# Kernel optimization log

Measured on AMD Instinct MI355X. Metric: run time of the kernel, lower is better.

Reference implementation:

```python
import jax, jax.numpy as jnp
import numpy as np
import math

N = 100000      # num vertices
M = 50000       # num hyperedges
NNZ = 800000    # incidence entries
F_IN = 128
NHID = 128
NCLS = 40
DEPTH = 4
ALPHA = 0.1     # restart_alpha
LAMDA = 0.5


def setup_inputs() -> dict:
    key = jax.random.key(0)
    ks = jax.random.split(key, 8)
    x = jax.random.normal(ks[0], (N, F_IN), jnp.float32)
    vertex = jax.random.randint(ks[1], (NNZ,), 0, N)
    edges = jax.random.randint(ks[2], (NNZ,), 0, M)
    s0 = 1.0 / np.sqrt(F_IN)
    sh = 1.0 / np.sqrt(NHID)
    W0 = jax.random.uniform(ks[3], (F_IN, NHID), jnp.float32, -s0, s0)
    b0 = jax.random.uniform(ks[4], (NHID,), jnp.float32, -s0, s0)
    Ws = jax.random.uniform(ks[5], (DEPTH, NHID, NHID), jnp.float32, -sh, sh)
    Wout = jax.random.uniform(ks[6], (NHID, NCLS), jnp.float32, -sh, sh)
    bout = jax.random.uniform(ks[7], (NCLS,), jnp.float32, -sh, sh)
    return {"x": x, "W0": W0, "b0": b0, "Ws": Ws, "Wout": Wout,
            "bout": bout, "vertex": vertex, "edges": edges}


def reference(x, W0, b0, Ws, Wout, bout, vertex, edges):
    ones = jnp.ones((NNZ, 1), x.dtype)
    cnt_e = jnp.maximum(jax.ops.segment_sum(ones, edges, num_segments=M), 1.0)
    cnt_v = jnp.maximum(jax.ops.segment_sum(ones, vertex, num_segments=N), 1.0)

    x = jax.nn.relu(x @ W0 + b0)
    x0 = x
    for i in range(DEPTH):
        beta = math.log(LAMDA / (i + 1) + 1.0)
        # vertex -> edge mean aggregation
        Xve = x[vertex]                                          # [NNZ, NHID]
        Xe = jax.ops.segment_sum(Xve, edges, num_segments=M) / cnt_e
        # edge -> vertex mean aggregation
        Xev = Xe[edges]                                          # [NNZ, NHID]
        Xv = jax.ops.segment_sum(Xev, vertex, num_segments=N) / cnt_v
        # L2 row-normalize with detached scale (use_norm=True)
        norm = jnp.linalg.norm(Xv, axis=1, keepdims=True)
        scale = jax.lax.stop_gradient(jnp.where(norm > 0, 1.0 / norm, 0.0))
        Xv = Xv * scale
        # alpha/beta residual blend (UniGCNII)
        Xi = (1.0 - ALPHA) * Xv + ALPHA * x0
        x = jax.nn.relu((1.0 - beta) * Xi + beta * (Xi @ Ws[i]))
    return x @ Wout + bout
```

## Files before the change

### kernel.cpp

```cpp
#include <hip/hip_runtime.h>

#define NV 100000
#define NE 50000
#define NNZ_C 800000
#define CAP_E 64
#define CAP_V 48
#define NB_E 391
#define NB_V 782
#define CAPB_E 2560
#define CAPB_V 1408
#define OVF_CAP 810000
#define T_ITEMS 4096
#define N_TILES ((NNZ_C + T_ITEMS - 1) / T_ITEMS)

typedef unsigned int uint32;
typedef unsigned short u16;
typedef u16 u16x8 __attribute__((ext_vector_type(8)));
typedef short short8 __attribute__((ext_vector_type(8)));
typedef float floatx16 __attribute__((ext_vector_type(16)));

__device__ __forceinline__ float bf2f(u16 h) {
  return __uint_as_float(((uint32)h) << 16);
}
__device__ __forceinline__ u16 f2bf(float f) {
  uint32 u = __float_as_uint(f);
  u += 0x7FFF + ((u >> 16) & 1);
  return (u16)(u >> 16);
}


__global__ void zero_misc(int* __restrict__ cur, int n,
                          u16* __restrict__ dummyX, u16* __restrict__ dummyXe) {
  int i = blockIdx.x * blockDim.x + threadIdx.x;
  if (i < n) cur[i] = 0;
  if (i < 128) { dummyX[i] = 0; dummyXe[i] = 0; }
}


__global__ __launch_bounds__(256) void scatter_binned(const int* __restrict__ vertex,
                                                      const int* __restrict__ edges,
                                                      int* __restrict__ curE,
                                                      int* __restrict__ curV,
                                                      int* __restrict__ ovfCnt,
                                                      uint32* __restrict__ pairE,
                                                      uint32* __restrict__ pairV,
                                                      uint2* __restrict__ ovfE,
                                                      uint2* __restrict__ ovfV) {
  __shared__ int histE[NB_E], baseE[NB_E];
  __shared__ int histV[NB_V], baseV[NB_V];
  int t = threadIdx.x;
  for (int tile = blockIdx.x; tile < N_TILES; tile += gridDim.x) {
    for (int b = t; b < NB_E; b += 256) histE[b] = 0;
    for (int b = t; b < NB_V; b += 256) histV[b] = 0;
    __syncthreads();
    int base = tile * T_ITEMS;
    int ev[16], vv[16], rE[16], rV[16];
    #pragma unroll
    for (int i = 0; i < 16; i++) {
      int k = base + t + i * 256;
      if (k < NNZ_C) {
        ev[i] = edges[k];
        vv[i] = vertex[k];
        rE[i] = atomicAdd(&histE[ev[i] >> 7], 1);
        rV[i] = atomicAdd(&histV[vv[i] >> 7], 1);
      }
    }
    __syncthreads();
    for (int b = t; b < NB_E; b += 256) {
      int h = histE[b];
      baseE[b] = h ? atomicAdd(&curE[b], h) : 0;
    }
    for (int b = t; b < NB_V; b += 256) {
      int h = histV[b];
      baseV[b] = h ? atomicAdd(&curV[b], h) : 0;
    }
    __syncthreads();
    #pragma unroll
    for (int i = 0; i < 16; i++) {
      int k = base + t + i * 256;
      if (k < NNZ_C) {
        uint32 e = (uint32)ev[i], v = (uint32)vv[i];
        uint32 pkE = ((e & 127u) << 25) | v;
        uint32 pkV = ((v & 127u) << 25) | e;
        int pE = baseE[e >> 7] + rE[i];
        if (pE < CAPB_E) pairE[(size_t)(e >> 7) * CAPB_E + pE] = pkE;
        else { int op = atomicAdd(&ovfCnt[0], 1); if (op < OVF_CAP) ovfE[op] = make_uint2(e >> 7, pkE); }
        int pV = baseV[v >> 7] + rV[i];
        if (pV < CAPB_V) pairV[(size_t)(v >> 7) * CAPB_V + pV] = pkV;
        else { int op = atomicAdd(&ovfCnt[1], 1); if (op < OVF_CAP) ovfV[op] = make_uint2(v >> 7, pkV); }
      }
    }
    __syncthreads();
  }
}

__global__ __launch_bounds__(256) void expand(const uint32* __restrict__ pairs,
                                              const int* __restrict__ cur, int capb,
                                              const uint2* __restrict__ ovf,
                                              const int* __restrict__ ovfCnt,
                                              int* __restrict__ items, int cap,
                                              int* __restrict__ cnt, int nKeys,
                                              int P, int dummy) {
  __shared__ int lcnt[128];
  int b = blockIdx.x, t = threadIdx.x;
  if (t < 128) lcnt[t] = 0;
  __syncthreads();
  int n = min(cur[b], capb);
  const uint32* p = pairs + (size_t)b * capb;
  for (int i = t; i < n; i += 256) {
    uint32 w = p[i];
    int loc = w >> 25;
    int val = (int)(w & 0x1FFFFFFu);
    int r = atomicAdd(&lcnt[loc], 1);
    if (r < cap) items[(size_t)((b << 7) + loc) * cap + r] = val;
  }
  int novf = min(*ovfCnt, OVF_CAP);
  for (int i = t; i < novf; i += 256) {
    uint2 w = ovf[i];
    if ((int)w.x == b) {
      int loc = w.y >> 25;
      int val = (int)(w.y & 0x1FFFFFFu);
      int r = atomicAdd(&lcnt[loc], 1);
      if (r < cap) items[(size_t)((b << 7) + loc) * cap + r] = val;
    }
  }
  __syncthreads();
  if (t < 128) {
    int key = (b << 7) + t;
    if (key < nKeys) {
      int c = lcnt[t];
      cnt[key] = c;
      int cc = min(c, cap);
      int padded = min((cc + P - 1) & ~(P - 1), cap);
      for (int r = cc; r < padded; r++)
        items[(size_t)key * cap + r] = dummy;
    }
  }
}


__global__ void prep_weights(const float* __restrict__ W0, const float* __restrict__ Ws,
                             u16* __restrict__ WT) {
  int idx = blockIdx.x * blockDim.x + threadIdx.x;
  if (idx >= 5 * 16384) return;
  const float betas[4] = {0.4054651081f, 0.2231435513f, 0.1541506798f, 0.1177830357f};
  int sec = idx >> 14;
  int rc = idx & 16383;
  int n = rc >> 7, k = rc & 127;
  float v;
  if (sec == 0) {
    v = W0[k * 128 + n];
  } else {
    int i = sec - 1;
    float b = betas[i];
    v = b * Ws[i * 16384 + k * 128 + n];
    if (k == n) v += 1.0f - b;
  }
  WT[idx] = f2bf(v);
}


__global__ __launch_bounds__(256) void edge_agg(const u16* __restrict__ Xh,
                                                const int* __restrict__ cntE,
                                                const int* __restrict__ itemsE,
                                                u16* __restrict__ Xeh) {
  int g = threadIdx.x >> 4;
  int lane = threadIdx.x & 15;
  int e = blockIdx.x * 16 + g;
  int cnt = cntE[e];
  int n16 = (min(cnt, CAP_E) + 15) & ~15;
  const int* it = itemsE + (size_t)e * CAP_E;
  float acc[8] = {0.f, 0.f, 0.f, 0.f, 0.f, 0.f, 0.f, 0.f};
  for (int j = 0; j < n16; j += 16) {
    int4 i0 = *(const int4*)(it + j);
    int4 i1 = *(const int4*)(it + j + 4);
    int4 i2 = *(const int4*)(it + j + 8);
    int4 i3 = *(const int4*)(it + j + 12);
    u16x8 r0 = *(const u16x8*)(Xh + (size_t)i0.x * 128 + lane * 8);
    u16x8 r1 = *(const u16x8*)(Xh + (size_t)i0.y * 128 + lane * 8);
    u16x8 r2 = *(const u16x8*)(Xh + (size_t)i0.z * 128 + lane * 8);
    u16x8 r3 = *(const u16x8*)(Xh + (size_t)i0.w * 128 + lane * 8);
    u16x8 r4 = *(const u16x8*)(Xh + (size_t)i1.x * 128 + lane * 8);
    u16x8 r5 = *(const u16x8*)(Xh + (size_t)i1.y * 128 + lane * 8);
    u16x8 r6 = *(const u16x8*)(Xh + (size_t)i1.z * 128 + lane * 8);
    u16x8 r7 = *(const u16x8*)(Xh + (size_t)i1.w * 128 + lane * 8);
    u16x8 r8 = *(const u16x8*)(Xh + (size_t)i2.x * 128 + lane * 8);
    u16x8 r9 = *(const u16x8*)(Xh + (size_t)i2.y * 128 + lane * 8);
    u16x8 rA = *(const u16x8*)(Xh + (size_t)i2.z * 128 + lane * 8);
    u16x8 rB = *(const u16x8*)(Xh + (size_t)i2.w * 128 + lane * 8);
    u16x8 rC = *(const u16x8*)(Xh + (size_t)i3.x * 128 + lane * 8);
    u16x8 rD = *(const u16x8*)(Xh + (size_t)i3.y * 128 + lane * 8);
    u16x8 rE = *(const u16x8*)(Xh + (size_t)i3.z * 128 + lane * 8);
    u16x8 rF = *(const u16x8*)(Xh + (size_t)i3.w * 128 + lane * 8);
    #pragma unroll
    for (int q = 0; q < 8; q++) {
      float s0 = (bf2f(r0[q]) + bf2f(r1[q])) + (bf2f(r2[q]) + bf2f(r3[q]));
      float s1 = (bf2f(r4[q]) + bf2f(r5[q])) + (bf2f(r6[q]) + bf2f(r7[q]));
      float s2 = (bf2f(r8[q]) + bf2f(r9[q])) + (bf2f(rA[q]) + bf2f(rB[q]));
      float s3 = (bf2f(rC[q]) + bf2f(rD[q])) + (bf2f(rE[q]) + bf2f(rF[q]));
      acc[q] += (s0 + s1) + (s2 + s3);
    }
  }
  float inv = 1.f / fmaxf((float)cnt, 1.f);
  u16x8 o;
  #pragma unroll
  for (int q = 0; q < 8; q++) o[q] = f2bf(acc[q] * inv);
  *(u16x8*)(Xeh + (size_t)e * 128 + lane * 8) = o;
}


__global__ __launch_bounds__(256, 5) void gemm_fused(const u16* __restrict__ Xeh,
                                                     const int* __restrict__ cntV,
                                                     const int* __restrict__ itemsV,
                                                     const u16* __restrict__ x0h,
                                                     const u16* __restrict__ WT,
                                                     u16* __restrict__ Yh, int nrows) {
  __shared__ u16 As[64 * 136];
  int t = threadIdx.x;
  int row0 = blockIdx.x * 64;
  int g = t >> 4, lane = t & 15;
  #pragma unroll
  for (int pass = 0; pass < 4; pass++) {
    int r = pass * 16 + g;
    int v = row0 + r;
    float acc[8] = {0.f, 0.f, 0.f, 0.f, 0.f, 0.f, 0.f, 0.f};
    int cnt = 0;
    if (v < nrows) {
      cnt = cntV[v];
      int n8 = (min(cnt, CAP_V) + 7) & ~7;
      const int* it = itemsV + (size_t)v * CAP_V;
      for (int j = 0; j < n8; j += 8) {
        int4 e0 = *(const int4*)(it + j);
        int4 e1 = *(const int4*)(it + j + 4);
        u16x8 r0 = *(const u16x8*)(Xeh + (size_t)e0.x * 128 + lane * 8);
        u16x8 r1 = *(const u16x8*)(Xeh + (size_t)e0.y * 128 + lane * 8);
        u16x8 r2 = *(const u16x8*)(Xeh + (size_t)e0.z * 128 + lane * 8);
        u16x8 r3 = *(const u16x8*)(Xeh + (size_t)e0.w * 128 + lane * 8);
        u16x8 r4 = *(const u16x8*)(Xeh + (size_t)e1.x * 128 + lane * 8);
        u16x8 r5 = *(const u16x8*)(Xeh + (size_t)e1.y * 128 + lane * 8);
        u16x8 r6 = *(const u16x8*)(Xeh + (size_t)e1.z * 128 + lane * 8);
        u16x8 r7 = *(const u16x8*)(Xeh + (size_t)e1.w * 128 + lane * 8);
        #pragma unroll
        for (int q = 0; q < 8; q++)
          acc[q] += ((bf2f(r0[q]) + bf2f(r1[q])) + (bf2f(r2[q]) + bf2f(r3[q]))) +
                    ((bf2f(r4[q]) + bf2f(r5[q])) + (bf2f(r6[q]) + bf2f(r7[q])));
      }
    }
    float inv = 1.f / fmaxf((float)cnt, 1.f);
    float sq = 0.f;
    #pragma unroll
    for (int q = 0; q < 8; q++) { acc[q] *= inv; sq += acc[q] * acc[q]; }
    sq += __shfl_xor(sq, 1, 64);
    sq += __shfl_xor(sq, 2, 64);
    sq += __shfl_xor(sq, 4, 64);
    sq += __shfl_xor(sq, 8, 64);
    float scale = (sq > 0.f) ? rsqrtf(sq) : 0.f;
    u16x8 o = {0, 0, 0, 0, 0, 0, 0, 0};
    if (v < nrows) {
      u16x8 x0v = *(const u16x8*)(x0h + (size_t)v * 128 + lane * 8);
      #pragma unroll
      for (int q = 0; q < 8; q++)
        o[q] = f2bf(0.9f * acc[q] * scale + 0.1f * bf2f(x0v[q]));
    }
    *(u16x8*)&As[r * 136 + lane * 8] = o;
  }
  __syncthreads();

  int w = t >> 6, lane64 = t & 63;
  int l31 = lane64 & 31, kh = lane64 >> 5;
  int wr = w >> 1, wc = w & 1;
  floatx16 acc[2];
  #pragma unroll
  for (int ct = 0; ct < 2; ct++)
    #pragma unroll
    for (int q = 0; q < 16; q++) acc[ct][q] = 0.f;

  const u16* wtb0 = WT + (size_t)(wc * 64 + l31) * 128;
  const u16* wtb1 = WT + (size_t)(wc * 64 + 32 + l31) * 128;
  #pragma unroll
  for (int ks = 0; ks < 8; ks++) {
    int koff = ks * 16 + kh * 8;
    short8 b0 = *(const short8*)(wtb0 + koff);
    short8 b1 = *(const short8*)(wtb1 + koff);
    short8 a0 = *(const short8*)&As[(wr * 32 + l31) * 136 + koff];
    acc[0] = __builtin_amdgcn_mfma_f32_32x32x16_bf16(a0, b0, acc[0], 0, 0, 0);
    acc[1] = __builtin_amdgcn_mfma_f32_32x32x16_bf16(a0, b1, acc[1], 0, 0, 0);
  }
  __syncthreads();

  #pragma unroll
  for (int ct = 0; ct < 2; ct++) {
    int col = wc * 64 + ct * 32 + l31;
    #pragma unroll
    for (int reg = 0; reg < 16; reg++) {
      int row = wr * 32 + (reg & 3) + 8 * (reg >> 2) + 4 * kh;
      As[row * 136 + col] = f2bf(fmaxf(acc[ct][reg], 0.f));
    }
  }
  __syncthreads();
  #pragma unroll
  for (int i = 0; i < 4; i++) {
    int idx = t + 256 * i;
    int r = idx >> 4, c8 = idx & 15;
    if (row0 + r < nrows)
      *(u16x8*)(Yh + (size_t)(row0 + r) * 128 + c8 * 8) =
          *(const u16x8*)&As[r * 136 + c8 * 8];
  }
}

__global__ __launch_bounds__(256, 4) void gemm_first(const float* __restrict__ A,
                                                     const u16* __restrict__ WT,
                                                     const float* __restrict__ bias,
                                                     u16* __restrict__ Yh,
                                                     u16* __restrict__ Y2h, int nrows) {
  __shared__ u16 As[128 * 136];
  int t = threadIdx.x;
  int row0 = blockIdx.x * 128;
  #pragma unroll
  for (int i = 0; i < 8; i++) {
    int idx = t + 256 * i;
    int r = idx >> 4, c8 = idx & 15;
    u16x8 v = {0, 0, 0, 0, 0, 0, 0, 0};
    if (row0 + r < nrows) {
      const float* p = A + (size_t)(row0 + r) * 128 + c8 * 8;
      float4 a = *(const float4*)p;
      float4 b = *(const float4*)(p + 4);
      v[0] = f2bf(a.x); v[1] = f2bf(a.y); v[2] = f2bf(a.z); v[3] = f2bf(a.w);
      v[4] = f2bf(b.x); v[5] = f2bf(b.y); v[6] = f2bf(b.z); v[7] = f2bf(b.w);
    }
    *(u16x8*)&As[r * 136 + c8 * 8] = v;
  }
  __syncthreads();

  int w = t >> 6, lane = t & 63;
  int l31 = lane & 31, kh = lane >> 5;
  int wr = w >> 1, wc = w & 1;
  floatx16 acc[2][2];
  #pragma unroll
  for (int rt = 0; rt < 2; rt++)
    #pragma unroll
    for (int ct = 0; ct < 2; ct++)
      #pragma unroll
      for (int q = 0; q < 16; q++) acc[rt][ct][q] = 0.f;

  const u16* wtb0 = WT + (size_t)(wc * 64 + l31) * 128;
  const u16* wtb1 = WT + (size_t)(wc * 64 + 32 + l31) * 128;
  #pragma unroll
  for (int ks = 0; ks < 8; ks++) {
    int koff = ks * 16 + kh * 8;
    short8 b0 = *(const short8*)(wtb0 + koff);
    short8 b1 = *(const short8*)(wtb1 + koff);
    short8 a0 = *(const short8*)&As[(wr * 64 + l31) * 136 + koff];
    short8 a1 = *(const short8*)&As[(wr * 64 + 32 + l31) * 136 + koff];
    acc[0][0] = __builtin_amdgcn_mfma_f32_32x32x16_bf16(a0, b0, acc[0][0], 0, 0, 0);
    acc[0][1] = __builtin_amdgcn_mfma_f32_32x32x16_bf16(a0, b1, acc[0][1], 0, 0, 0);
    acc[1][0] = __builtin_amdgcn_mfma_f32_32x32x16_bf16(a1, b0, acc[1][0], 0, 0, 0);
    acc[1][1] = __builtin_amdgcn_mfma_f32_32x32x16_bf16(a1, b1, acc[1][1], 0, 0, 0);
  }
  __syncthreads();

  #pragma unroll
  for (int rt = 0; rt < 2; rt++)
    #pragma unroll
    for (int ct = 0; ct < 2; ct++) {
      int col = wc * 64 + ct * 32 + l31;
      float bv = bias[col];
      #pragma unroll
      for (int reg = 0; reg < 16; reg++) {
        int row = wr * 64 + rt * 32 + (reg & 3) + 8 * (reg >> 2) + 4 * kh;
        As[row * 136 + col] = f2bf(fmaxf(acc[rt][ct][reg] + bv, 0.f));
      }
    }
  __syncthreads();
  #pragma unroll
  for (int i = 0; i < 8; i++) {
    int idx = t + 256 * i;
    int r = idx >> 4, c8 = idx & 15;
    if (row0 + r < nrows) {
      u16x8 v = *(const u16x8*)&As[r * 136 + c8 * 8];
      *(u16x8*)(Yh + (size_t)(row0 + r) * 128 + c8 * 8) = v;
      *(u16x8*)(Y2h + (size_t)(row0 + r) * 128 + c8 * 8) = v;
    }
  }
}


__global__ __launch_bounds__(256) void gemm_out(const u16* __restrict__ Xh,
                                                const float* __restrict__ W,
                                                const float* __restrict__ bias,
                                                float* __restrict__ Y, int nrows) {
  __shared__ float xs[128][36];
  __shared__ float ws[32][44];
  int t = threadIdx.x;
  int tr = t >> 3;
  int tc = t & 7;
  int row0 = blockIdx.x * 128;
  float acc[4][5];
  #pragma unroll
  for (int i = 0; i < 4; i++)
    #pragma unroll
    for (int j = 0; j < 5; j++) acc[i][j] = 0.f;

  for (int k0 = 0; k0 < 128; k0 += 32) {
    #pragma unroll
    for (int i = 0; i < 2; i++) {
      int idx = t + 256 * i;
      int r = idx >> 2, c8 = idx & 3;
      int gr = row0 + r;
      u16x8 v = {0, 0, 0, 0, 0, 0, 0, 0};
      if (gr < nrows) v = *(const u16x8*)(Xh + (size_t)gr * 128 + k0 + c8 * 8);
      #pragma unroll
      for (int q = 0; q < 8; q++) xs[r][c8 * 8 + q] = bf2f(v[q]);
    }
    #pragma unroll
    for (int i = 0; i < 5; i++) {
      int idx = t + 256 * i;
      int r = idx / 40, c = idx % 40;
      ws[r][c] = W[(k0 + r) * 40 + c];
    }
    __syncthreads();
    #pragma unroll
    for (int kk4 = 0; kk4 < 8; kk4++) {
      float4 xv[4];
      #pragma unroll
      for (int i = 0; i < 4; i++) xv[i] = *(const float4*)&xs[tr + 32 * i][kk4 * 4];
      #pragma unroll
      for (int q = 0; q < 4; q++) {
        int kk = kk4 * 4 + q;
        float wv[5];
        #pragma unroll
        for (int j = 0; j < 5; j++) wv[j] = ws[kk][tc * 5 + j];
        #pragma unroll
        for (int i = 0; i < 4; i++) {
          float xq = ((const float*)&xv[i])[q];
          #pragma unroll
          for (int j = 0; j < 5; j++) acc[i][j] += xq * wv[j];
        }
      }
    }
    __syncthreads();
  }
  #pragma unroll
  for (int i = 0; i < 4; i++) {
    int gr = row0 + tr + 32 * i;
    if (gr >= nrows) continue;
    #pragma unroll
    for (int j = 0; j < 5; j++) {
      int c = tc * 5 + j;
      Y[(long)gr * 40 + c] = acc[i][j] + bias[c];
    }
  }
}


extern "C" void kernel_launch(void* const* d_in, const int* in_sizes, int n_in,
                              void* d_out, int out_size, void* d_ws, size_t ws_size,
                              hipStream_t stream) {
  const float* x    = (const float*)d_in[0];
  const float* W0   = (const float*)d_in[1];
  const float* b0   = (const float*)d_in[2];
  const float* Ws   = (const float*)d_in[3];
  const float* Wout = (const float*)d_in[4];
  const float* bout = (const float*)d_in[5];
  const int* vertex = (const int*)d_in[6];
  const int* edges  = (const int*)d_in[7];
  float* out = (float*)d_out;

  char* base = (char*)d_ws;
  size_t o = 0;
  auto alloc = [&](size_t bytes) -> char* {
    char* r = base + o;
    o += (bytes + 255) & ~(size_t)255;
    return r;
  };
  u16* x_curh = (u16*)alloc((size_t)(NV + 1) * 128 * 2);
  u16* x0h    = (u16*)alloc((size_t)NV * 128 * 2);
  u16* Xeh    = (u16*)alloc((size_t)(NE + 1) * 128 * 2);
  u16* WT     = (u16*)alloc((size_t)5 * 16384 * 2);
  int* cntE   = (int*)alloc((size_t)NE * 4);
  int* cntV   = (int*)alloc((size_t)NV * 4);
  int* itemsE = (int*)alloc((size_t)NE * CAP_E * 4);
  int* itemsV = (int*)alloc((size_t)NV * CAP_V * 4);
  uint32* pairE = (uint32*)alloc((size_t)NB_E * CAPB_E * 4);
  uint32* pairV = (uint32*)alloc((size_t)NB_V * CAPB_V * 4);
  uint2* ovfE  = (uint2*)alloc((size_t)OVF_CAP * 8);
  uint2* ovfV  = (uint2*)alloc((size_t)OVF_CAP * 8);
  int* curAll = (int*)alloc((size_t)(NB_E + NB_V + 2) * 4);
  int* curE = curAll;
  int* curV = curAll + NB_E;
  int* ovfCnt = curAll + NB_E + NB_V;

  int nzero = NB_E + NB_V + 2;
  zero_misc<<<(nzero + 255) / 256, 256, 0, stream>>>(curAll, nzero,
                                                     x_curh + (size_t)NV * 128,
                                                     Xeh + (size_t)NE * 128);
  scatter_binned<<<N_TILES, 256, 0, stream>>>(vertex, edges, curE, curV, ovfCnt,
                                              pairE, pairV, ovfE, ovfV);
  expand<<<NB_E, 256, 0, stream>>>(pairE, curE, CAPB_E, ovfE, ovfCnt,
                                   itemsE, CAP_E, cntE, NE, 16, NV);
  expand<<<NB_V, 256, 0, stream>>>(pairV, curV, CAPB_V, ovfV, ovfCnt + 1,
                                   itemsV, CAP_V, cntV, NV, 8, NE);
  prep_weights<<<(5 * 16384 + 255) / 256, 256, 0, stream>>>(W0, Ws, WT);

  int gblocks = (NV + 127) / 128;
  int fblocks = (NV + 63) / 64;
  gemm_first<<<gblocks, 256, 0, stream>>>(x, WT, b0, x_curh, x0h, NV);

  for (int i = 0; i < 4; i++) {
    edge_agg<<<NE / 16, 256, 0, stream>>>(x_curh, cntE, itemsE, Xeh);
    gemm_fused<<<fblocks, 256, 0, stream>>>(Xeh, cntV, itemsV, x0h,
                                            WT + (size_t)(1 + i) * 16384, x_curh, NV);
  }
  gemm_out<<<gblocks, 256, 0, stream>>>(x_curh, Wout, bout, out, NV);
}
```

Before: 481.0 us.

## Slice feature matrices into 16-column planes for cache-local gathers

Feature matrices move to a sliced layout of 8 planes, each holding 16 columns per row. Edge and vertex gathers then run per slice (blockIdx & 7), so each slice's working set (about 3.2MB for vertices) can stay in cache during the random gathers. The vertex aggregation is split out of the fused GEMM into its own kernel, which writes partial squared norms that the GEMM reduces. The cost is an extra kernel and an intermediate Xv buffer round-trip per layer. The index lists are also reread 8 times, once per slice.

```diff
diff --git a/kernel.cpp b/kernel.cpp
--- a/kernel.cpp
+++ b/kernel.cpp
@@ -12,6 +12,8 @@
 #define OVF_CAP 810000
 #define T_ITEMS 4096
 #define N_TILES ((NNZ_C + T_ITEMS - 1) / T_ITEMS)
+#define ET (NB_E)
+#define VT (NB_V)
 
 typedef unsigned int uint32;
 typedef unsigned short u16;
@@ -30,10 +32,14 @@
 
 
 __global__ void zero_misc(int* __restrict__ cur, int n,
-                          u16* __restrict__ dummyX, u16* __restrict__ dummyXe) {
+                          u16* __restrict__ Xcs, u16* __restrict__ Xes) {
   int i = blockIdx.x * blockDim.x + threadIdx.x;
   if (i < n) cur[i] = 0;
-  if (i < 128) { dummyX[i] = 0; dummyXe[i] = 0; }
+  if (i < 128) {
+    int s = i >> 4, j = i & 15;
+    Xcs[((size_t)s * (NV + 1) + NV) * 16 + j] = 0;
+    Xes[((size_t)s * (NE + 1) + NE) * 16 + j] = 0;
+  }
 }
 
 
@@ -160,38 +166,42 @@
 }
 
 
-__global__ __launch_bounds__(256) void edge_agg(const u16* __restrict__ Xh,
-                                                const int* __restrict__ cntE,
-                                                const int* __restrict__ itemsE,
-                                                u16* __restrict__ Xeh) {
-  int g = threadIdx.x >> 4;
-  int lane = threadIdx.x & 15;
-  int e = blockIdx.x * 16 + g;
+__global__ __launch_bounds__(256) void edge_agg_s(const u16* __restrict__ Xcs,
+                                                  const int* __restrict__ cntE,
+                                                  const int* __restrict__ itemsE,
+                                                  u16* __restrict__ Xes) {
+  int s = blockIdx.x & 7;
+  int tile = blockIdx.x >> 3;
+  int t = threadIdx.x;
+  int p = t >> 1, half = t & 1;
+  int e = tile * 128 + p;
+  if (e >= NE) return;
   int cnt = cntE[e];
   int n16 = (min(cnt, CAP_E) + 15) & ~15;
   const int* it = itemsE + (size_t)e * CAP_E;
+  const u16* src = Xcs + (size_t)s * (NV + 1) * 16 + half * 8;
   float acc[8] = {0.f, 0.f, 0.f, 0.f, 0.f, 0.f, 0.f, 0.f};
   for (int j = 0; j < n16; j += 16) {
     int4 i0 = *(const int4*)(it + j);
     int4 i1 = *(const int4*)(it + j + 4);
     int4 i2 = *(const int4*)(it + j + 8);
     int4 i3 = *(const int4*)(it + j + 12);
-    u16x8 r0 = *(const u16x8*)(Xh + (size_t)i0.x * 128 + lane * 8);
-    u16x8 r1 = *(const u16x8*)(Xh + (size_t)i0.y * 128 + lane * 8);
-    u16x8 r2 = *(const u16x8*)(Xh + (size_t)i0.z * 128 + lane * 8);
-    u16x8 r3 = *(const u16x8*)(Xh + (size_t)i0.w * 128 + lane * 8);
-    u16x8 r4 = *(const u16x8*)(Xh + (size_t)i1.x * 128 + lane * 8);
-    u16x8 r5 = *(const u16x8*)(Xh + (size_t)i1.y * 128 + lane * 8);
-    u16x8 r6 = *(const u16x8*)(Xh + (size_t)i1.z * 128 + lane * 8);
-    u16x8 r7 = *(const u16x8*)(Xh + (size_t)i1.w * 128 + lane * 8);
-    u16x8 r8 = *(const u16x8*)(Xh + (size_t)i2.x * 128 + lane * 8);
-    u16x8 r9 = *(const u16x8*)(Xh + (size_t)i2.y * 128 + lane * 8);
-    u16x8 rA = *(const u16x8*)(Xh + (size_t)i2.z * 128 + lane * 8);
-    u16x8 rB = *(const u16x8*)(Xh + (size_t)i2.w * 128 + lane * 8);
-    u16x8 rC = *(const u16x8*)(Xh + (size_t)i3.x * 128 + lane * 8);
-    u16x8 rD = *(const u16x8*)(Xh + (size_t)i3.y * 128 + lane * 8);
-    u16x8 rE = *(const u16x8*)(Xh + (size_t)i3.z * 128 + lane * 8);
-    u16x8 rF = *(const u16x8*)(Xh + (size_t)i3.w * 128 + lane * 8);
+    u16x8 r0 = *(const u16x8*)(src + (size_t)i0.x * 16);
+    u16x8 r1 = *(const u16x8*)(src + (size_t)i0.y * 16);
+    u16x8 r2 = *(const u16x8*)(src + (size_t)i0.z * 16);
+    u16x8 r3 = *(const u16x8*)(src + (size_t)i0.w * 16);
+    u16x8 r4 = *(const u16x8*)(src + (size_t)i1.x * 16);
+    u16x8 r5 = *(const u16x8*)(src + (size_t)i1.y * 16);
+    u16x8 r6 = *(const u16x8*)(src + (size_t)i1.z * 16);
+    u16x8 r7 = *(const u16x8*)(src + (size_t)i1.w * 16);
+    u16x8 r8 = *(const u16x8*)(src + (size_t)i2.x * 16);
+    u16x8 r9 = *(const u16x8*)(src + (size_t)i2.y * 16);
+    u16x8 rA = *(const u16x8*)(src + (size_t)i2.z * 16);
+    u16x8 rB = *(const u16x8*)(src + (size_t)i2.w * 16);
+    u16x8 rC = *(const u16x8*)(src + (size_t)i3.x * 16);
+    u16x8 rD = *(const u16x8*)(src + (size_t)i3.y * 16);
+    u16x8 rE = *(const u16x8*)(src + (size_t)i3.z * 16);
+    u16x8 rF = *(const u16x8*)(src + (size_t)i3.w * 16);
     #pragma unroll
     for (int q = 0; q < 8; q++) {
       float s0 = (bf2f(r0[q]) + bf2f(r1[q])) + (bf2f(r2[q]) + bf2f(r3[q]));
@@ -205,63 +215,90 @@
   u16x8 o;
   #pragma unroll
   for (int q = 0; q < 8; q++) o[q] = f2bf(acc[q] * inv);
-  *(u16x8*)(Xeh + (size_t)e * 128 + lane * 8) = o;
-}
-
-
-__global__ __launch_bounds__(256, 5) void gemm_fused(const u16* __restrict__ Xeh,
-                                                     const int* __restrict__ cntV,
-                                                     const int* __restrict__ itemsV,
-                                                     const u16* __restrict__ x0h,
-                                                     const u16* __restrict__ WT,
-                                                     u16* __restrict__ Yh, int nrows) {
+  *(u16x8*)(Xes + ((size_t)s * (NE + 1) + e) * 16 + half * 8) = o;
+}
+
+
+__global__ __launch_bounds__(256) void vertex_gather_s(const u16* __restrict__ Xes,
+                                                       const int* __restrict__ cntV,
+                                                       const int* __restrict__ itemsV,
+                                                       u16* __restrict__ Xvs,
+                                                       float* __restrict__ nb) {
+  int s = blockIdx.x & 7;
+  int tile = blockIdx.x >> 3;
+  int t = threadIdx.x;
+  int p = t >> 1, half = t & 1;
+  int v = tile * 128 + p;
+  if (v >= NV) return;
+  int cnt = cntV[v];
+  int n8 = (min(cnt, CAP_V) + 7) & ~7;
+  const int* it = itemsV + (size_t)v * CAP_V;
+  const u16* src = Xes + (size_t)s * (NE + 1) * 16 + half * 8;
+  float acc[8] = {0.f, 0.f, 0.f, 0.f, 0.f, 0.f, 0.f, 0.f};
+  for (int j = 0; j < n8; j += 8) {
+    int4 e0 = *(const int4*)(it + j);
+    int4 e1 = *(const int4*)(it + j + 4);
+    u16x8 r0 = *(const u16x8*)(src + (size_t)e0.x * 16);
+    u16x8 r1 = *(const u16x8*)(src + (size_t)e0.y * 16);
+    u16x8 r2 = *(const u16x8*)(src + (size_t)e0.z * 16);
+    u16x8 r3 = *(const u16x8*)(src + (size_t)e0.w * 16);
+    u16x8 r4 = *(const u16x8*)(src + (size_t)e1.x * 16);
+    u16x8 r5 = *(const u16x8*)(src + (size_t)e1.y * 16);
+    u16x8 r6 = *(const u16x8*)(src + (size_t)e1.z * 16);
+    u16x8 r7 = *(const u16x8*)(src + (size_t)e1.w * 16);
+    #pragma unroll
+    for (int q = 0; q < 8; q++)
+      acc[q] += ((bf2f(r0[q]) + bf2f(r1[q])) + (bf2f(r2[q]) + bf2f(r3[q]))) +
+                ((bf2f(r4[q]) + bf2f(r5[q])) + (bf2f(r6[q]) + bf2f(r7[q])));
+  }
+  float inv = 1.f / fmaxf((float)cnt, 1.f);
+  u16x8 o;
+  float sq = 0.f;
+  #pragma unroll
+  for (int q = 0; q < 8; q++) {
+    o[q] = f2bf(acc[q] * inv);
+    float m = bf2f(o[q]);
+    sq += m * m;
+  }
+  sq += __shfl_xor(sq, 1, 64);
+  if (half == 0) nb[(size_t)s * NV + v] = sq;
+  *(u16x8*)(Xvs + ((size_t)s * NV + v) * 16 + half * 8) = o;
+}
+
+
+__global__ __launch_bounds__(256, 5) void gemm_norm(const u16* __restrict__ Xvs,
+                                                    const float* __restrict__ nb,
+                                                    const u16* __restrict__ x0s,
+                                                    const u16* __restrict__ WT,
+                                                    u16* __restrict__ Xcs, int nrows) {
   __shared__ u16 As[64 * 136];
   int t = threadIdx.x;
   int row0 = blockIdx.x * 64;
   int g = t >> 4, lane = t & 15;
+  int sl = lane >> 1, half = lane & 1;
   #pragma unroll
   for (int pass = 0; pass < 4; pass++) {
     int r = pass * 16 + g;
     int v = row0 + r;
-    float acc[8] = {0.f, 0.f, 0.f, 0.f, 0.f, 0.f, 0.f, 0.f};
-    int cnt = 0;
+    u16x8 mv = {0, 0, 0, 0, 0, 0, 0, 0};
+    u16x8 x0v = {0, 0, 0, 0, 0, 0, 0, 0};
+    float nbv = 0.f;
     if (v < nrows) {
-      cnt = cntV[v];
-      int n8 = (min(cnt, CAP_V) + 7) & ~7;
-      const int* it = itemsV + (size_t)v * CAP_V;
-      for (int j = 0; j < n8; j += 8) {
-        int4 e0 = *(const int4*)(it + j);
-        int4 e1 = *(const int4*)(it + j + 4);
-        u16x8 r0 = *(const u16x8*)(Xeh + (size_t)e0.x * 128 + lane * 8);
-        u16x8 r1 = *(const u16x8*)(Xeh + (size_t)e0.y * 128 + lane * 8);
-        u16x8 r2 = *(const u16x8*)(Xeh + (size_t)e0.z * 128 + lane * 8);
-        u16x8 r3 = *(const u16x8*)(Xeh + (size_t)e0.w * 128 + lane * 8);
-        u16x8 r4 = *(const u16x8*)(Xeh + (size_t)e1.x * 128 + lane * 8);
-        u16x8 r5 = *(const u16x8*)(Xeh + (size_t)e1.y * 128 + lane * 8);
-        u16x8 r6 = *(const u16x8*)(Xeh + (size_t)e1.z * 128 + lane * 8);
-        u16x8 r7 = *(const u16x8*)(Xeh + (size_t)e1.w * 128 + lane * 8);
-        #pragma unroll
-        for (int q = 0; q < 8; q++)
-          acc[q] += ((bf2f(r0[q]) + bf2f(r1[q])) + (bf2f(r2[q]) + bf2f(r3[q]))) +
-                    ((bf2f(r4[q]) + bf2f(r5[q])) + (bf2f(r6[q]) + bf2f(r7[q])));
-      }
-    }
-    float inv = 1.f / fmaxf((float)cnt, 1.f);
-    float sq = 0.f;
-    #pragma unroll
-    for (int q = 0; q < 8; q++) { acc[q] *= inv; sq += acc[q] * acc[q]; }
+      size_t off = ((size_t)sl * NV + v) * 16 + half * 8;
+      mv = *(const u16x8*)(Xvs + off);
+      x0v = *(const u16x8*)(x0s + off);
+      nbv = (lane < 8) ? nb[(size_t)lane * NV + v] : 0.f;
+    }
+    float sq = nbv;
     sq += __shfl_xor(sq, 1, 64);
     sq += __shfl_xor(sq, 2, 64);
     sq += __shfl_xor(sq, 4, 64);
     sq += __shfl_xor(sq, 8, 64);
     float scale = (sq > 0.f) ? rsqrtf(sq) : 0.f;
-    u16x8 o = {0, 0, 0, 0, 0, 0, 0, 0};
-    if (v < nrows) {
-      u16x8 x0v = *(const u16x8*)(x0h + (size_t)v * 128 + lane * 8);
-      #pragma unroll
-      for (int q = 0; q < 8; q++)
-        o[q] = f2bf(0.9f * acc[q] * scale + 0.1f * bf2f(x0v[q]));
-    }
+    u16x8 o;
+    #pragma unroll
+    for (int q = 0; q < 8; q++)
+      o[q] = f2bf(0.9f * bf2f(mv[q]) * scale + 0.1f * bf2f(x0v[q]));
     *(u16x8*)&As[r * 136 + lane * 8] = o;
   }
   __syncthreads();
@@ -303,7 +340,7 @@
     int idx = t + 256 * i;
     int r = idx >> 4, c8 = idx & 15;
     if (row0 + r < nrows)
-      *(u16x8*)(Yh + (size_t)(row0 + r) * 128 + c8 * 8) =
+      *(u16x8*)(Xcs + ((size_t)(c8 >> 1) * (NV + 1) + row0 + r) * 16 + (c8 & 1) * 8) =
           *(const u16x8*)&As[r * 136 + c8 * 8];
   }
 }
@@ -311,8 +348,8 @@
 __global__ __launch_bounds__(256, 4) void gemm_first(const float* __restrict__ A,
                                                      const u16* __restrict__ WT,
                                                      const float* __restrict__ bias,
-                                                     u16* __restrict__ Yh,
-                                                     u16* __restrict__ Y2h, int nrows) {
+                                                     u16* __restrict__ Xcs,
+                                                     u16* __restrict__ x0s, int nrows) {
   __shared__ u16 As[128 * 136];
   int t = threadIdx.x;
   int row0 = blockIdx.x * 128;
@@ -378,14 +415,15 @@
     int r = idx >> 4, c8 = idx & 15;
     if (row0 + r < nrows) {
       u16x8 v = *(const u16x8*)&As[r * 136 + c8 * 8];
-      *(u16x8*)(Yh + (size_t)(row0 + r) * 128 + c8 * 8) = v;
-      *(u16x8*)(Y2h + (size_t)(row0 + r) * 128 + c8 * 8) = v;
-    }
-  }
-}
-
-
-__global__ __launch_bounds__(256) void gemm_out(const u16* __restrict__ Xh,
+      int sl = c8 >> 1, hf = c8 & 1;
+      *(u16x8*)(Xcs + ((size_t)sl * (NV + 1) + row0 + r) * 16 + hf * 8) = v;
+      *(u16x8*)(x0s + ((size_t)sl * NV + row0 + r) * 16 + hf * 8) = v;
+    }
+  }
+}
+
+
+__global__ __launch_bounds__(256) void gemm_out(const u16* __restrict__ Xcs,
                                                 const float* __restrict__ W,
                                                 const float* __restrict__ bias,
                                                 float* __restrict__ Y, int nrows) {
@@ -408,7 +446,10 @@
       int r = idx >> 2, c8 = idx & 3;
       int gr = row0 + r;
       u16x8 v = {0, 0, 0, 0, 0, 0, 0, 0};
-      if (gr < nrows) v = *(const u16x8*)(Xh + (size_t)gr * 128 + k0 + c8 * 8);
+      if (gr < nrows) {
+        int f = k0 + c8 * 8;
+        v = *(const u16x8*)(Xcs + ((size_t)(f >> 4) * (NV + 1) + gr) * 16 + (f & 15));
+      }
       #pragma unroll
       for (int q = 0; q < 8; q++) xs[r][c8 * 8 + q] = bf2f(v[q]);
     }
@@ -473,10 +514,12 @@
     o += (bytes + 255) & ~(size_t)255;
     return r;
   };
-  u16* x_curh = (u16*)alloc((size_t)(NV + 1) * 128 * 2);
-  u16* x0h    = (u16*)alloc((size_t)NV * 128 * 2);
-  u16* Xeh    = (u16*)alloc((size_t)(NE + 1) * 128 * 2);
-  u16* WT     = (u16*)alloc((size_t)5 * 16384 * 2);
+  u16* Xcs  = (u16*)alloc((size_t)8 * (NV + 1) * 16 * 2);
+  u16* x0s  = (u16*)alloc((size_t)8 * NV * 16 * 2);
+  u16* Xes  = (u16*)alloc((size_t)8 * (NE + 1) * 16 * 2);
+  u16* Xvs  = (u16*)alloc((size_t)8 * NV * 16 * 2);
+  float* nbuf = (float*)alloc((size_t)8 * NV * 4);
+  u16* WT   = (u16*)alloc((size_t)5 * 16384 * 2);
   int* cntE   = (int*)alloc((size_t)NE * 4);
   int* cntV   = (int*)alloc((size_t)NV * 4);
   int* itemsE = (int*)alloc((size_t)NE * CAP_E * 4);
@@ -491,9 +534,7 @@
   int* ovfCnt = curAll + NB_E + NB_V;
 
   int nzero = NB_E + NB_V + 2;
-  zero_misc<<<(nzero + 255) / 256, 256, 0, stream>>>(curAll, nzero,
-                                                     x_curh + (size_t)NV * 128,
-                                                     Xeh + (size_t)NE * 128);
+  zero_misc<<<(nzero + 255) / 256, 256, 0, stream>>>(curAll, nzero, Xcs, Xes);
   scatter_binned<<<N_TILES, 256, 0, stream>>>(vertex, edges, curE, curV, ovfCnt,
                                               pairE, pairV, ovfE, ovfV);
   expand<<<NB_E, 256, 0, stream>>>(pairE, curE, CAPB_E, ovfE, ovfCnt,
@@ -504,12 +545,13 @@
 
   int gblocks = (NV + 127) / 128;
   int fblocks = (NV + 63) / 64;
-  gemm_first<<<gblocks, 256, 0, stream>>>(x, WT, b0, x_curh, x0h, NV);
+  gemm_first<<<gblocks, 256, 0, stream>>>(x, WT, b0, Xcs, x0s, NV);
 
   for (int i = 0; i < 4; i++) {
-    edge_agg<<<NE / 16, 256, 0, stream>>>(x_curh, cntE, itemsE, Xeh);
-    gemm_fused<<<fblocks, 256, 0, stream>>>(Xeh, cntV, itemsV, x0h,
-                                            WT + (size_t)(1 + i) * 16384, x_curh, NV);
-  }
-  gemm_out<<<gblocks, 256, 0, stream>>>(x_curh, Wout, bout, out, NV);
-}
+    edge_agg_s<<<ET * 8, 256, 0, stream>>>(Xcs, cntE, itemsE, Xes);
+    vertex_gather_s<<<VT * 8, 256, 0, stream>>>(Xes, cntV, itemsV, Xvs, nbuf);
+    gemm_norm<<<fblocks, 256, 0, stream>>>(Xvs, nbuf, x0s,
+                                           WT + (size_t)(1 + i) * 16384, Xcs, NV);
+  }
+  gemm_out<<<gblocks, 256, 0, stream>>>(Xcs, Wout, bout, out, NV);
+}
```

Result: slower. 629.6 us (+30.9%).
